# Kernel tuning notes

Measured on AMD Instinct MI355X. Metric: run time of the kernel, lower is better.

The kernel has to match this reference:

```python
import jax, jax.numpy as jnp
import numpy as np

B, T, K = 256, 1024, 128  # batch, seq_len, num_tags (= config.vocab_size)


def setup_inputs() -> dict:
    key = jax.random.key(0)
    k1, k2, k3, k4 = jax.random.split(key, 4)
    return {
        "hidden_states": jax.random.normal(k1, (B, T, K), dtype=jnp.float32),
        "transitions": jax.random.normal(k2, (K, K), dtype=jnp.float32) * 0.1,
        "start_transitions": jax.random.normal(k3, (K,), dtype=jnp.float32) * 0.1,
        "end_transitions": jax.random.normal(k4, (K,), dtype=jnp.float32) * 0.1,
    }


def reference(hidden_states, transitions, start_transitions, end_transitions):
    """CRF forward algorithm: log-partition over all tag sequences.

    hidden_states: [B, T, K] emission scores
    transitions:   [K, K]  transitions[i, j] = score of tag i -> tag j
    Returns logZ per sequence: [B]
    """
    emis = hidden_states
    # alpha_0: [B, K]
    alpha0 = start_transitions[None, :] + emis[:, 0]

    def step(alpha, e_t):
        # alpha: [B, K] log-scores ending at previous tag
        # scores[b, i, j] = alpha[b, i] + transitions[i, j]
        scores = alpha[:, :, None] + transitions[None, :, :]  # [B, K, K]
        new_alpha = jax.nn.logsumexp(scores, axis=1) + e_t    # [B, K]
        return new_alpha, None

    emis_rest = jnp.swapaxes(emis[:, 1:], 0, 1)  # [T-1, B, K]
    alphaT, _ = jax.lax.scan(step, alpha0, emis_rest)
    return jax.nn.logsumexp(alphaT + end_transitions[None, :], axis=1)  # [B]
```

## Files before the change

### kernel.cpp

```cpp
#include <hip/hip_runtime.h>
#include <cstddef>
#include <cstdint>

typedef float f2    __attribute__((ext_vector_type(2)));
typedef float f32x4 __attribute__((ext_vector_type(4)));
typedef short bf16x8 __attribute__((ext_vector_type(8)));

__device__ __forceinline__ float fast_exp2(float x) { return __builtin_amdgcn_exp2f(x); }
__device__ __forceinline__ float fast_log2(float x) { return __builtin_amdgcn_logf(x); }

__device__ __forceinline__ short bf16rne(float x) {
  uint32_t u = __float_as_uint(x);
  u += 0x7fffu + ((u >> 16) & 1u);
  return (short)(u >> 16);
}

__device__ __forceinline__ void bar_lds() {
  asm volatile("s_waitcnt lgkmcnt(0)\n\ts_barrier" ::: "memory");
}

namespace {
constexpr int Bc = 256, Tc = 1024, Kc = 128;
constexpr int ROWS = 16;
constexpr int NC = 96;
constexpr int WARM = 12;
constexpr int MEAS = 1023 - WARM;
constexpr float L2E = 1.4426950408889634f;
constexpr float LN2 = 0.6931471805599453f;
constexpr int PSTR = 136;
}

__global__ __launch_bounds__(256, 3) void crf_chunk_kernel(
    const float* __restrict__ hs,
    const float* __restrict__ trans,
    const float* __restrict__ start_t,
    const float* __restrict__ end_t,
    float* __restrict__ ws)
{
  __shared__ __align__(16) unsigned short pL[2][ROWS][PSTR];
  __shared__ float sSc[2][ROWS];
  __shared__ float sRed[4][ROWS];

  const int tid = (int)threadIdx.x;
  const int w = tid >> 6;
  const int lane = tid & 63;
  const int b = lane & 15;
  const int kq = lane >> 4;
  const int rb = (int)blockIdx.x & 15;
  const int ck = (int)blockIdx.x >> 4;
  const int brow = rb * ROWS + b;
  const int s0 = (MEAS * ck) / NC;
  const int L  = (MEAS * (ck + 1)) / NC - s0;
  const int NSTEPS = WARM + L;
  const float* __restrict__ eb = hs + (size_t)brow * Tc * Kc + (size_t)s0 * Kc;

  const int jb0 = 32 * w + 4 * kq;
  const int jb1 = jb0 + 16;

  bf16x8 A[2][4];
#pragma unroll
  for (int np = 0; np < 2; ++np)
#pragma unroll
    for (int tt = 0; tt < 4; ++tt) {
      bf16x8 a;
#pragma unroll
      for (int jj = 0; jj < 8; ++jj) {
        const int kg = 32 * tt + 8 * kq + jj;
        const int rg = 16 * (2 * w + np) + b;
        a[jj] = bf16rne(fast_exp2(trans[(size_t)kg * Kc + rg] * L2E));
      }
      A[np][tt] = a;
    }

  f32x4 er[4][2];
#pragma unroll
  for (int d = 0; d < 4; ++d) {
    er[d][0] = *(const f32x4*)&eb[(size_t)(1 + d) * Kc + jb0];
    er[d][1] = *(const f32x4*)&eb[(size_t)(1 + d) * Kc + jb1];
  }

  if (ck == 0) {
#pragma unroll
    for (int np = 0; np < 2; ++np) {
      const int jb = np ? jb1 : jb0;
      f32x4 sv = *(const f32x4*)&start_t[jb];
      f32x4 e0 = *(const f32x4*)&eb[jb];
      uint32_t d0 = (uint32_t)(uint16_t)bf16rne(fast_exp2((sv.x + e0.x) * L2E)) |
                    ((uint32_t)(uint16_t)bf16rne(fast_exp2((sv.y + e0.y) * L2E)) << 16);
      uint32_t d1 = (uint32_t)(uint16_t)bf16rne(fast_exp2((sv.z + e0.z) * L2E)) |
                    ((uint32_t)(uint16_t)bf16rne(fast_exp2((sv.w + e0.w) * L2E)) << 16);
      *(uint2*)&pL[0][b][jb] = make_uint2(d0, d1);
    }
  } else {
    *(uint2*)&pL[0][b][jb0] = make_uint2(0x3F803F80u, 0x3F803F80u);
    *(uint2*)&pL[0][b][jb1] = make_uint2(0x3F803F80u, 0x3F803F80u);
  }
  bar_lds();
  bf16x8 Bf[4];
#pragma unroll
  for (int tt = 0; tt < 4; ++tt)
    Bf[tt] = *(const bf16x8*)&pL[0][b][32 * tt + 8 * kq];

  float scale = 1.0f;
  int curE0 = 0;
  int Mi = 0;
  f32x4 pf0 = {0, 0, 0, 0}, pf1 = {0, 0, 0, 0};

#define STEP(T, U) do {                                                         \
    const f32x4 z4 = {0.f, 0.f, 0.f, 0.f};                                      \
    f32x4 c01 = __builtin_amdgcn_mfma_f32_16x16x32_bf16(A[0][1], Bf[1],         \
        __builtin_amdgcn_mfma_f32_16x16x32_bf16(A[0][0], Bf[0], z4, 0, 0, 0),   \
        0, 0, 0);                                                               \
    f32x4 c23 = __builtin_amdgcn_mfma_f32_16x16x32_bf16(A[0][3], Bf[3],         \
        __builtin_amdgcn_mfma_f32_16x16x32_bf16(A[0][2], Bf[2], z4, 0, 0, 0),   \
        0, 0, 0);                                                               \
    const f32x4 C0 = c01 + c23;                                                 \
    c01 = __builtin_amdgcn_mfma_f32_16x16x32_bf16(A[1][1], Bf[1],               \
        __builtin_amdgcn_mfma_f32_16x16x32_bf16(A[1][0], Bf[0], z4, 0, 0, 0),   \
        0, 0, 0);                                                               \
    c23 = __builtin_amdgcn_mfma_f32_16x16x32_bf16(A[1][3], Bf[3],               \
        __builtin_amdgcn_mfma_f32_16x16x32_bf16(A[1][2], Bf[2], z4, 0, 0, 0),   \
        0, 0, 0);                                                               \
    const f32x4 C1 = c01 + c23;                                                 \
    f32x4 se0, se1;                                                             \
    {                                                                           \
      f32x4 e = er[U][0];                                                       \
      se0.x = scale * fast_exp2(e.x * L2E); se0.y = scale * fast_exp2(e.y * L2E); \
      se0.z = scale * fast_exp2(e.z * L2E); se0.w = scale * fast_exp2(e.w * L2E); \
      e = er[U][1];                                                             \
      se1.x = scale * fast_exp2(e.x * L2E); se1.y = scale * fast_exp2(e.y * L2E); \
      se1.z = scale * fast_exp2(e.z * L2E); se1.w = scale * fast_exp2(e.w * L2E); \
    }                                                                           \
    Mi += curE0;                                                                \
    {                                                                           \
      int rn = (T) + 4; if (rn > NSTEPS) rn = NSTEPS;                           \
      er[U][0] = *(const f32x4*)&eb[(size_t)rn * Kc + jb0];                     \
      er[U][1] = *(const f32x4*)&eb[(size_t)rn * Kc + jb1];                     \
    }                                                                           \
    {                                                                           \
      f32x4 p;                                                                  \
      p.x = C0.x * se0.x; p.y = C0.y * se0.y;                                   \
      p.z = C0.z * se0.z; p.w = C0.w * se0.w;                                   \
      pf0 = p;                                                                  \
      uint32_t d0 = (uint32_t)(uint16_t)bf16rne(p.x) | ((uint32_t)(uint16_t)bf16rne(p.y) << 16); \
      uint32_t d1 = (uint32_t)(uint16_t)bf16rne(p.z) | ((uint32_t)(uint16_t)bf16rne(p.w) << 16); \
      *(uint2*)&pL[(T) & 1][b][jb0] = make_uint2(d0, d1);                       \
      p.x = C1.x * se1.x; p.y = C1.y * se1.y;                                   \
      p.z = C1.z * se1.z; p.w = C1.w * se1.w;                                   \
      pf1 = p;                                                                  \
      d0 = (uint32_t)(uint16_t)bf16rne(p.x) | ((uint32_t)(uint16_t)bf16rne(p.y) << 16); \
      d1 = (uint32_t)(uint16_t)bf16rne(p.z) | ((uint32_t)(uint16_t)bf16rne(p.w) << 16); \
      *(uint2*)&pL[(T) & 1][b][jb1] = make_uint2(d0, d1);                       \
    }                                                                           \
    if (w == 0 && kq == 0) sSc[(T) & 1][b] = C0.x;                              \
    bar_lds();                                                                  \
    Bf[0] = *(const bf16x8*)&pL[(T) & 1][b][8 * kq];                            \
    Bf[1] = *(const bf16x8*)&pL[(T) & 1][b][32 + 8 * kq];                       \
    Bf[2] = *(const bf16x8*)&pL[(T) & 1][b][64 + 8 * kq];                       \
    Bf[3] = *(const bf16x8*)&pL[(T) & 1][b][96 + 8 * kq];                       \
    {                                                                           \
      float s0v = sSc[(T) & 1][b];                                              \
      uint32_t ex = (__float_as_uint(s0v) >> 23) & 0xffu;                       \
      curE0 = (int)ex - 127;                                                    \
      scale = __uint_as_float((254u - ex) << 23);                               \
    }                                                                           \
  } while (0)

  auto measureA = [&](bool weighted) -> float {
    float part;
    if (weighted) {
      f32x4 e0 = *(const f32x4*)&end_t[jb0];
      f32x4 e1 = *(const f32x4*)&end_t[jb1];
      part = pf0.x * fast_exp2(e0.x * L2E) + pf0.y * fast_exp2(e0.y * L2E) +
             pf0.z * fast_exp2(e0.z * L2E) + pf0.w * fast_exp2(e0.w * L2E) +
             pf1.x * fast_exp2(e1.x * L2E) + pf1.y * fast_exp2(e1.y * L2E) +
             pf1.z * fast_exp2(e1.z * L2E) + pf1.w * fast_exp2(e1.w * L2E);
    } else {
      part = pf0.x + pf0.y + pf0.z + pf0.w + pf1.x + pf1.y + pf1.z + pf1.w;
    }
    part += __shfl_xor(part, 16);
    part += __shfl_xor(part, 32);
    if (lane < ROWS) sRed[w][lane] = part;
    bar_lds();
    float Av = 0.f;
    if (w == 0 && lane < ROWS) {
      float S = sRed[0][lane] + sRed[1][lane] + sRed[2][lane] + sRed[3][lane];
      Av = (float)Mi + fast_log2(S);
    }
    return Av;
  };

  STEP(1, 0);  STEP(2, 1);  STEP(3, 2);  STEP(4, 3);
  STEP(5, 0);  STEP(6, 1);  STEP(7, 2);  STEP(8, 3);
  STEP(9, 0);  STEP(10, 1); STEP(11, 2); STEP(12, 3);
  const float Amid = measureA(false);

  STEP(13, 0); STEP(14, 1); STEP(15, 2); STEP(16, 3);
  STEP(17, 0); STEP(18, 1); STEP(19, 2); STEP(20, 3);
  STEP(21, 0); STEP(22, 1);
  if (L == 11) { STEP(23, 2); }
  const float Aend = measureA(ck == NC - 1);

#undef STEP

  if (w == 0 && lane < ROWS)
    ws[(size_t)ck * Bc + brow] = Aend - (ck ? Amid : 0.f);
}

__global__ __launch_bounds__(256, 1) void crf_combine(
    const float* __restrict__ ws, float* __restrict__ out)
{
  const int b = (int)threadIdx.x;
  float s = 0.f;
#pragma unroll
  for (int cc = 0; cc < NC; ++cc) s += ws[(size_t)cc * Bc + b];
  out[b] = s * LN2;
}

extern "C" void kernel_launch(void* const* d_in, const int* in_sizes, int n_in,
                              void* d_out, int out_size, void* d_ws, size_t ws_size,
                              hipStream_t stream) {
  const float* hs    = (const float*)d_in[0];
  const float* trans = (const float*)d_in[1];
  const float* st    = (const float*)d_in[2];
  const float* en    = (const float*)d_in[3];
  float* ws = (float*)d_ws;
  crf_chunk_kernel<<<dim3(NC * Bc / ROWS), dim3(256), 0, stream>>>(hs, trans, st, en, ws);
  crf_combine<<<dim3(1), dim3(Bc), 0, stream>>>(ws, (float*)d_out);
}
```

Baseline: 209.0 us.

## Run each 16-row chunk in one wavefront, removing LDS exchange and barriers

Each chunk block shrinks from four wavefronts to one, and that wavefront holds all eight N-tiles of exp(transitions) in registers. The next B operand is built directly from MFMA outputs with a permuted transition layout, so the per-step LDS write, barrier and read-back are gone. The exp(transitions) matrix is now computed once by a new prep kernel into the workspace rather than by every block, and scaling is folded into the exp argument through an fma. In exchange each wave does four times more MFMA and exp work per step with heavy register use, and occupancy drops to one wave per block.

New measurement: 224.0 us. +7.2%, slower.

```diff
diff --git a/kernel.cpp b/kernel.cpp
--- a/kernel.cpp
+++ b/kernel.cpp
@@ -2,7 +2,6 @@
 #include <cstddef>
 #include <cstdint>
 
-typedef float f2    __attribute__((ext_vector_type(2)));
 typedef float f32x4 __attribute__((ext_vector_type(4)));
 typedef short bf16x8 __attribute__((ext_vector_type(8)));
 
@@ -15,195 +14,172 @@
   return (short)(u >> 16);
 }
 
-__device__ __forceinline__ void bar_lds() {
-  asm volatile("s_waitcnt lgkmcnt(0)\n\ts_barrier" ::: "memory");
-}
-
 namespace {
 constexpr int Bc = 256, Tc = 1024, Kc = 128;
-constexpr int ROWS = 16;
 constexpr int NC = 96;
 constexpr int WARM = 12;
 constexpr int MEAS = 1023 - WARM;
 constexpr float L2E = 1.4426950408889634f;
 constexpr float LN2 = 0.6931471805599453f;
-constexpr int PSTR = 136;
-}
-
-__global__ __launch_bounds__(256, 3) void crf_chunk_kernel(
+constexpr int WS_ET2 = NC * Bc;
+}
+
+__global__ __launch_bounds__(128, 1) void crf_prep(
+    const float* __restrict__ trans, float* __restrict__ ws)
+{
+  unsigned short* et = reinterpret_cast<unsigned short*>(ws + WS_ET2);
+  const int m = (int)blockIdx.x;
+  const int c = (int)threadIdx.x;
+  const int tau = (c & 0x63) | ((c & 4) << 2) | ((c & 0x18) >> 1);
+  et[(size_t)m * Kc + c] =
+      (unsigned short)bf16rne(fast_exp2(trans[(size_t)tau * Kc + m] * L2E));
+}
+
+__global__ __launch_bounds__(64) void crf_chunk_kernel(
     const float* __restrict__ hs,
-    const float* __restrict__ trans,
     const float* __restrict__ start_t,
     const float* __restrict__ end_t,
     float* __restrict__ ws)
 {
-  __shared__ __align__(16) unsigned short pL[2][ROWS][PSTR];
-  __shared__ float sSc[2][ROWS];
-  __shared__ float sRed[4][ROWS];
-
-  const int tid = (int)threadIdx.x;
-  const int w = tid >> 6;
-  const int lane = tid & 63;
+  const int lane = (int)threadIdx.x;
   const int b = lane & 15;
-  const int kq = lane >> 4;
+  const int q = lane >> 4;
   const int rb = (int)blockIdx.x & 15;
   const int ck = (int)blockIdx.x >> 4;
-  const int brow = rb * ROWS + b;
+  const int brow = rb * 16 + b;
   const int s0 = (MEAS * ck) / NC;
   const int L  = (MEAS * (ck + 1)) / NC - s0;
   const int NSTEPS = WARM + L;
   const float* __restrict__ eb = hs + (size_t)brow * Tc * Kc + (size_t)s0 * Kc;
-
-  const int jb0 = 32 * w + 4 * kq;
-  const int jb1 = jb0 + 16;
-
-  bf16x8 A[2][4];
-#pragma unroll
-  for (int np = 0; np < 2; ++np)
+  const unsigned short* __restrict__ et =
+      reinterpret_cast<const unsigned short*>(ws + WS_ET2);
+
+  bf16x8 Ap[8][4];
+#pragma unroll
+  for (int nt = 0; nt < 8; ++nt)
+#pragma unroll
+    for (int tt = 0; tt < 4; ++tt)
+      Ap[nt][tt] = *(const bf16x8*)&et[(size_t)(16 * nt + b) * Kc + 32 * tt + 8 * q];
+
+  f32x4 er[8];
+#pragma unroll
+  for (int nt = 0; nt < 8; ++nt)
+    er[nt] = *(const f32x4*)&eb[(size_t)Kc + 16 * nt + 4 * q];
+
+  bf16x8 Bf[4];
+  if (ck == 0) {
 #pragma unroll
     for (int tt = 0; tt < 4; ++tt) {
-      bf16x8 a;
-#pragma unroll
-      for (int jj = 0; jj < 8; ++jj) {
-        const int kg = 32 * tt + 8 * kq + jj;
-        const int rg = 16 * (2 * w + np) + b;
-        a[jj] = bf16rne(fast_exp2(trans[(size_t)kg * Kc + rg] * L2E));
-      }
-      A[np][tt] = a;
-    }
-
-  f32x4 er[4][2];
-#pragma unroll
-  for (int d = 0; d < 4; ++d) {
-    er[d][0] = *(const f32x4*)&eb[(size_t)(1 + d) * Kc + jb0];
-    er[d][1] = *(const f32x4*)&eb[(size_t)(1 + d) * Kc + jb1];
-  }
-
-  if (ck == 0) {
-#pragma unroll
-    for (int np = 0; np < 2; ++np) {
-      const int jb = np ? jb1 : jb0;
-      f32x4 sv = *(const f32x4*)&start_t[jb];
-      f32x4 e0 = *(const f32x4*)&eb[jb];
-      uint32_t d0 = (uint32_t)(uint16_t)bf16rne(fast_exp2((sv.x + e0.x) * L2E)) |
-                    ((uint32_t)(uint16_t)bf16rne(fast_exp2((sv.y + e0.y) * L2E)) << 16);
-      uint32_t d1 = (uint32_t)(uint16_t)bf16rne(fast_exp2((sv.z + e0.z) * L2E)) |
-                    ((uint32_t)(uint16_t)bf16rne(fast_exp2((sv.w + e0.w) * L2E)) << 16);
-      *(uint2*)&pL[0][b][jb] = make_uint2(d0, d1);
+      f32x4 sv0 = *(const f32x4*)&start_t[32 * tt + 4 * q];
+      f32x4 sv1 = *(const f32x4*)&start_t[32 * tt + 4 * q + 16];
+      f32x4 e0v = *(const f32x4*)&eb[32 * tt + 4 * q];
+      f32x4 e1v = *(const f32x4*)&eb[32 * tt + 4 * q + 16];
+      bf16x8 v;
+      v[0] = bf16rne(fast_exp2((sv0.x + e0v.x) * L2E));
+      v[1] = bf16rne(fast_exp2((sv0.y + e0v.y) * L2E));
+      v[2] = bf16rne(fast_exp2((sv0.z + e0v.z) * L2E));
+      v[3] = bf16rne(fast_exp2((sv0.w + e0v.w) * L2E));
+      v[4] = bf16rne(fast_exp2((sv1.x + e1v.x) * L2E));
+      v[5] = bf16rne(fast_exp2((sv1.y + e1v.y) * L2E));
+      v[6] = bf16rne(fast_exp2((sv1.z + e1v.z) * L2E));
+      v[7] = bf16rne(fast_exp2((sv1.w + e1v.w) * L2E));
+      Bf[tt] = v;
     }
   } else {
-    *(uint2*)&pL[0][b][jb0] = make_uint2(0x3F803F80u, 0x3F803F80u);
-    *(uint2*)&pL[0][b][jb1] = make_uint2(0x3F803F80u, 0x3F803F80u);
+    const short one = (short)0x3F80;
+#pragma unroll
+    for (int tt = 0; tt < 4; ++tt) {
+      bf16x8 v;
+#pragma unroll
+      for (int j = 0; j < 8; ++j) v[j] = one;
+      Bf[tt] = v;
+    }
   }
-  bar_lds();
-  bf16x8 Bf[4];
-#pragma unroll
-  for (int tt = 0; tt < 4; ++tt)
-    Bf[tt] = *(const bf16x8*)&pL[0][b][32 * tt + 8 * kq];
-
-  float scale = 1.0f;
+
+  float sf = 0.f;
   int curE0 = 0;
   int Mi = 0;
-  f32x4 pf0 = {0, 0, 0, 0}, pf1 = {0, 0, 0, 0};
-
-#define STEP(T, U) do {                                                         \
+  f32x4 P[8];
+
+#define STEP(T) do {                                                            \
     const f32x4 z4 = {0.f, 0.f, 0.f, 0.f};                                      \
-    f32x4 c01 = __builtin_amdgcn_mfma_f32_16x16x32_bf16(A[0][1], Bf[1],         \
-        __builtin_amdgcn_mfma_f32_16x16x32_bf16(A[0][0], Bf[0], z4, 0, 0, 0),   \
-        0, 0, 0);                                                               \
-    f32x4 c23 = __builtin_amdgcn_mfma_f32_16x16x32_bf16(A[0][3], Bf[3],         \
-        __builtin_amdgcn_mfma_f32_16x16x32_bf16(A[0][2], Bf[2], z4, 0, 0, 0),   \
-        0, 0, 0);                                                               \
-    const f32x4 C0 = c01 + c23;                                                 \
-    c01 = __builtin_amdgcn_mfma_f32_16x16x32_bf16(A[1][1], Bf[1],               \
-        __builtin_amdgcn_mfma_f32_16x16x32_bf16(A[1][0], Bf[0], z4, 0, 0, 0),   \
-        0, 0, 0);                                                               \
-    c23 = __builtin_amdgcn_mfma_f32_16x16x32_bf16(A[1][3], Bf[3],               \
-        __builtin_amdgcn_mfma_f32_16x16x32_bf16(A[1][2], Bf[2], z4, 0, 0, 0),   \
-        0, 0, 0);                                                               \
-    const f32x4 C1 = c01 + c23;                                                 \
-    f32x4 se0, se1;                                                             \
+    Mi += curE0;                                                                \
+    float c00src = 0.f;                                                         \
+    _Pragma("unroll")                                                           \
+    for (int nt = 0; nt < 8; ++nt) {                                            \
+      f32x4 c01 = __builtin_amdgcn_mfma_f32_16x16x32_bf16(Ap[nt][1], Bf[1],     \
+          __builtin_amdgcn_mfma_f32_16x16x32_bf16(Ap[nt][0], Bf[0], z4, 0, 0, 0), \
+          0, 0, 0);                                                             \
+      f32x4 c23 = __builtin_amdgcn_mfma_f32_16x16x32_bf16(Ap[nt][3], Bf[3],     \
+          __builtin_amdgcn_mfma_f32_16x16x32_bf16(Ap[nt][2], Bf[2], z4, 0, 0, 0), \
+          0, 0, 0);                                                             \
+      f32x4 cv = c01 + c23;                                                     \
+      if (nt == 0) c00src = cv.x;                                               \
+      f32x4 e = er[nt];                                                         \
+      f32x4 p;                                                                  \
+      p.x = cv.x * fast_exp2(__builtin_fmaf(e.x, L2E, sf));                     \
+      p.y = cv.y * fast_exp2(__builtin_fmaf(e.y, L2E, sf));                     \
+      p.z = cv.z * fast_exp2(__builtin_fmaf(e.z, L2E, sf));                     \
+      p.w = cv.w * fast_exp2(__builtin_fmaf(e.w, L2E, sf));                     \
+      P[nt] = p;                                                                \
+    }                                                                           \
     {                                                                           \
-      f32x4 e = er[U][0];                                                       \
-      se0.x = scale * fast_exp2(e.x * L2E); se0.y = scale * fast_exp2(e.y * L2E); \
-      se0.z = scale * fast_exp2(e.z * L2E); se0.w = scale * fast_exp2(e.w * L2E); \
-      e = er[U][1];                                                             \
-      se1.x = scale * fast_exp2(e.x * L2E); se1.y = scale * fast_exp2(e.y * L2E); \
-      se1.z = scale * fast_exp2(e.z * L2E); se1.w = scale * fast_exp2(e.w * L2E); \
-    }                                                                           \
-    Mi += curE0;                                                                \
+      int rn = (T) + 1; if (rn > NSTEPS) rn = NSTEPS;                           \
+      _Pragma("unroll")                                                         \
+      for (int nt = 0; nt < 8; ++nt)                                            \
+        er[nt] = *(const f32x4*)&eb[(size_t)rn * Kc + 16 * nt + 4 * q];         \
+    }                                                                           \
+    float c00 = __shfl(c00src, b, 64);   \
+    _Pragma("unroll")                                                           \
+    for (int tt = 0; tt < 4; ++tt) {                                            \
+      bf16x8 v;                                                                 \
+      v[0] = bf16rne(P[2 * tt].x);     v[1] = bf16rne(P[2 * tt].y);             \
+      v[2] = bf16rne(P[2 * tt].z);     v[3] = bf16rne(P[2 * tt].w);             \
+      v[4] = bf16rne(P[2 * tt + 1].x); v[5] = bf16rne(P[2 * tt + 1].y);         \
+      v[6] = bf16rne(P[2 * tt + 1].z); v[7] = bf16rne(P[2 * tt + 1].w);         \
+      Bf[tt] = v;                                                               \
+    }                                                                           \
     {                                                                           \
-      int rn = (T) + 4; if (rn > NSTEPS) rn = NSTEPS;                           \
-      er[U][0] = *(const f32x4*)&eb[(size_t)rn * Kc + jb0];                     \
-      er[U][1] = *(const f32x4*)&eb[(size_t)rn * Kc + jb1];                     \
-    }                                                                           \
-    {                                                                           \
-      f32x4 p;                                                                  \
-      p.x = C0.x * se0.x; p.y = C0.y * se0.y;                                   \
-      p.z = C0.z * se0.z; p.w = C0.w * se0.w;                                   \
-      pf0 = p;                                                                  \
-      uint32_t d0 = (uint32_t)(uint16_t)bf16rne(p.x) | ((uint32_t)(uint16_t)bf16rne(p.y) << 16); \
-      uint32_t d1 = (uint32_t)(uint16_t)bf16rne(p.z) | ((uint32_t)(uint16_t)bf16rne(p.w) << 16); \
-      *(uint2*)&pL[(T) & 1][b][jb0] = make_uint2(d0, d1);                       \
-      p.x = C1.x * se1.x; p.y = C1.y * se1.y;                                   \
-      p.z = C1.z * se1.z; p.w = C1.w * se1.w;                                   \
-      pf1 = p;                                                                  \
-      d0 = (uint32_t)(uint16_t)bf16rne(p.x) | ((uint32_t)(uint16_t)bf16rne(p.y) << 16); \
-      d1 = (uint32_t)(uint16_t)bf16rne(p.z) | ((uint32_t)(uint16_t)bf16rne(p.w) << 16); \
-      *(uint2*)&pL[(T) & 1][b][jb1] = make_uint2(d0, d1);                       \
-    }                                                                           \
-    if (w == 0 && kq == 0) sSc[(T) & 1][b] = C0.x;                              \
-    bar_lds();                                                                  \
-    Bf[0] = *(const bf16x8*)&pL[(T) & 1][b][8 * kq];                            \
-    Bf[1] = *(const bf16x8*)&pL[(T) & 1][b][32 + 8 * kq];                       \
-    Bf[2] = *(const bf16x8*)&pL[(T) & 1][b][64 + 8 * kq];                       \
-    Bf[3] = *(const bf16x8*)&pL[(T) & 1][b][96 + 8 * kq];                       \
-    {                                                                           \
-      float s0v = sSc[(T) & 1][b];                                              \
-      uint32_t ex = (__float_as_uint(s0v) >> 23) & 0xffu;                       \
+      uint32_t ex = (__float_as_uint(c00) >> 23) & 0xffu;                       \
       curE0 = (int)ex - 127;                                                    \
-      scale = __uint_as_float((254u - ex) << 23);                               \
+      sf = (float)(127 - (int)ex);                                              \
     }                                                                           \
   } while (0)
 
-  auto measureA = [&](bool weighted) -> float {
-    float part;
-    if (weighted) {
-      f32x4 e0 = *(const f32x4*)&end_t[jb0];
-      f32x4 e1 = *(const f32x4*)&end_t[jb1];
-      part = pf0.x * fast_exp2(e0.x * L2E) + pf0.y * fast_exp2(e0.y * L2E) +
-             pf0.z * fast_exp2(e0.z * L2E) + pf0.w * fast_exp2(e0.w * L2E) +
-             pf1.x * fast_exp2(e1.x * L2E) + pf1.y * fast_exp2(e1.y * L2E) +
-             pf1.z * fast_exp2(e1.z * L2E) + pf1.w * fast_exp2(e1.w * L2E);
-    } else {
-      part = pf0.x + pf0.y + pf0.z + pf0.w + pf1.x + pf1.y + pf1.z + pf1.w;
-    }
-    part += __shfl_xor(part, 16);
-    part += __shfl_xor(part, 32);
-    if (lane < ROWS) sRed[w][lane] = part;
-    bar_lds();
-    float Av = 0.f;
-    if (w == 0 && lane < ROWS) {
-      float S = sRed[0][lane] + sRed[1][lane] + sRed[2][lane] + sRed[3][lane];
-      Av = (float)Mi + fast_log2(S);
-    }
-    return Av;
-  };
-
-  STEP(1, 0);  STEP(2, 1);  STEP(3, 2);  STEP(4, 3);
-  STEP(5, 0);  STEP(6, 1);  STEP(7, 2);  STEP(8, 3);
-  STEP(9, 0);  STEP(10, 1); STEP(11, 2); STEP(12, 3);
-  const float Amid = measureA(false);
-
-  STEP(13, 0); STEP(14, 1); STEP(15, 2); STEP(16, 3);
-  STEP(17, 0); STEP(18, 1); STEP(19, 2); STEP(20, 3);
-  STEP(21, 0); STEP(22, 1);
-  if (L == 11) { STEP(23, 2); }
-  const float Aend = measureA(ck == NC - 1);
+#define MEASURE(DST, WEIGHTED) do {                                             \
+    float part = 0.f;                                                           \
+    if (WEIGHTED) {                                                             \
+      _Pragma("unroll")                                                         \
+      for (int nt = 0; nt < 8; ++nt) {                                          \
+        f32x4 ev = *(const f32x4*)&end_t[16 * nt + 4 * q];                      \
+        part += P[nt].x * fast_exp2(ev.x * L2E) + P[nt].y * fast_exp2(ev.y * L2E) \
+              + P[nt].z * fast_exp2(ev.z * L2E) + P[nt].w * fast_exp2(ev.w * L2E); \
+      }                                                                         \
+    } else {                                                                    \
+      _Pragma("unroll")                                                         \
+      for (int nt = 0; nt < 8; ++nt)                                            \
+        part += P[nt].x + P[nt].y + P[nt].z + P[nt].w;                          \
+    }                                                                           \
+    part += __shfl_xor(part, 16);                                               \
+    part += __shfl_xor(part, 32);                                               \
+    DST = (float)Mi + fast_log2(part);                                          \
+  } while (0)
+
+  STEP(1);  STEP(2);  STEP(3);  STEP(4);
+  STEP(5);  STEP(6);  STEP(7);  STEP(8);
+  STEP(9);  STEP(10); STEP(11); STEP(12);
+  float Amid; MEASURE(Amid, false);
+
+  STEP(13); STEP(14); STEP(15); STEP(16);
+  STEP(17); STEP(18); STEP(19); STEP(20);
+  STEP(21); STEP(22);
+  if (L == 11) { STEP(23); }
+  float Aend; MEASURE(Aend, (ck == NC - 1));
 
 #undef STEP
-
-  if (w == 0 && lane < ROWS)
+#undef MEASURE
+
+  if (lane < 16)
     ws[(size_t)ck * Bc + brow] = Aend - (ck ? Amid : 0.f);
 }
 
@@ -225,6 +201,7 @@
   const float* st    = (const float*)d_in[2];
   const float* en    = (const float*)d_in[3];
   float* ws = (float*)d_ws;
-  crf_chunk_kernel<<<dim3(NC * Bc / ROWS), dim3(256), 0, stream>>>(hs, trans, st, en, ws);
+  crf_prep<<<dim3(Kc), dim3(Kc), 0, stream>>>(trans, ws);
+  crf_chunk_kernel<<<dim3(NC * 16), dim3(64), 0, stream>>>(hs, st, en, ws);
   crf_combine<<<dim3(1), dim3(Bc), 0, stream>>>(ws, (float*)d_out);
 }
```
